# Kernel optimization log

Measured on AMD Instinct MI355X. Metric: run time of the kernel, lower is better.

## Reference

```python
import jax, jax.numpy as jnp
import numpy as np

B, L, D = 4, 4096, 1024
H, HD = 16, 64          # num_heads, head_dims
K = 256                 # Linformer low-rank dim
SCALE = HD ** -0.5


def setup_inputs() -> dict:
    key = jax.random.key(0)
    ks = jax.random.split(key, 7)
    std_d = 1.0 / np.sqrt(D)
    std_k = 1.0 / np.sqrt(K)
    return {
        "x": jax.random.normal(ks[0], (B, L, D), dtype=jnp.float32),
        "Wq": jax.random.uniform(ks[1], (D, D), jnp.float32, -std_d, std_d),
        "Wk": jax.random.uniform(ks[2], (D, D), jnp.float32, -std_d, std_d),
        "Wv": jax.random.uniform(ks[3], (D, D), jnp.float32, -std_d, std_d),
        "Wo": jax.random.uniform(ks[4], (D, D), jnp.float32, -std_d, std_d),
        "proj_k": jax.random.uniform(ks[5], (L, K), jnp.float32, -std_k, std_k),
        "proj_v": jax.random.uniform(ks[6], (L, K), jnp.float32, -std_k, std_k),
    }


def reference(x, Wq, Wk, Wv, Wo, proj_k, proj_v):
    # QKV projections (bias-free linears)
    q = x @ Wq                                   # [B, L, D]
    k = x @ Wk                                   # [B, L, D]
    v = x @ Wv                                   # [B, L, D]
    # Linformer low-rank projection along sequence: 'bld,lk->bkd'
    k = jnp.einsum('bld,lk->bkd', k, proj_k)     # [B, K, D]
    v = jnp.einsum('bld,lk->bkd', v, proj_v)     # [B, K, D]
    # split heads
    q = q.reshape(B, L, H, HD).transpose(0, 2, 1, 3)   # [B, H, L, HD]
    k = k.reshape(B, K, H, HD).transpose(0, 2, 1, 3)   # [B, H, K, HD]
    v = v.reshape(B, K, H, HD).transpose(0, 2, 1, 3)   # [B, H, K, HD]
    # attention over compressed length K
    logits = jnp.einsum('bhld,bhkd->bhlk', q, k) * SCALE   # [B, H, L, K]
    attn = jax.nn.softmax(logits, axis=-1)
    out = jnp.einsum('bhlk,bhkd->bhld', attn, v)           # [B, H, L, HD]
    out = out.transpose(0, 2, 1, 3).reshape(B, L, H * HD)  # [B, L, D]
    return out @ Wo
```

## Files before the change

kernel.cpp:

```cpp
#include <hip/hip_runtime.h>
#include <stdint.h>

typedef __bf16 bf16;
typedef __bf16 bf16x4 __attribute__((ext_vector_type(4)));
typedef __bf16 bf16x8 __attribute__((ext_vector_type(8)));
typedef float f32x4 __attribute__((ext_vector_type(4)));

__global__ __launch_bounds__(256) void k_castT(const float* __restrict__ src,
                                               bf16* __restrict__ dst,
                                               bf16* __restrict__ dstT) {
  const size_t bo = (size_t)blockIdx.z * 4096 * 1024;
  const float* s = src + bo;
  bf16* d = dst + bo;
  bf16* dT = dstT + bo;
  __shared__ float tile[64][65];
  const int r0 = blockIdx.y * 64, c0 = blockIdx.x * 64;
  const int tr = threadIdx.x >> 6, tc = threadIdx.x & 63;
#pragma unroll
  for (int i = 0; i < 16; ++i) {
    const int r = i * 4 + tr;
    const float v = s[(size_t)(r0 + r) * 1024 + (c0 + tc)];
    tile[r][tc] = v;
    d[(size_t)(r0 + r) * 1024 + (c0 + tc)] = (bf16)v;
  }
  __syncthreads();
#pragma unroll
  for (int i = 0; i < 16; ++i) {
    const int r = i * 4 + tr;
    dT[(size_t)(c0 + r) * 4096 + (r0 + tc)] = (bf16)tile[tc][r];
  }
}

struct TP4 { const float* src[4]; bf16* dst[4]; };

__global__ __launch_bounds__(256) void k_tcast(TP4 args, int R, int C) {
  const float* __restrict__ src = args.src[blockIdx.z];
  bf16* __restrict__ dst = args.dst[blockIdx.z];
  __shared__ float tile[64][65];
  const int r0 = blockIdx.y * 64, c0 = blockIdx.x * 64;
  const int tr = threadIdx.x >> 6, tc = threadIdx.x & 63;
#pragma unroll
  for (int i = 0; i < 16; ++i) {
    int r = i * 4 + tr;
    tile[r][tc] = src[(size_t)(r0 + r) * C + (c0 + tc)];
  }
  __syncthreads();
#pragma unroll
  for (int i = 0; i < 16; ++i) {
    int r = i * 4 + tr;
    dst[(size_t)(c0 + r) * R + (r0 + tc)] = (bf16)tile[tc][r];
  }
}

#define GLL(gp, lp)                                              \
  __builtin_amdgcn_global_load_lds(                              \
      (const __attribute__((address_space(1))) void*)(gp),       \
      (__attribute__((address_space(3))) void*)(lp), 16, 0, 0)

template <typename CT>
__global__ __launch_bounds__(256) void k_gemm_nt(
    const bf16* __restrict__ A, const bf16* __restrict__ Bt,
    const bf16* __restrict__ Bt2, CT* __restrict__ C,
    int lda, int ldb, int ldc, int Kd, long sA, long sB, long sC,
    int zmod, long kOff, int mbSplit, CT* __restrict__ Ct, long sCt, int ldct,
    int mbT) {
  int zb = blockIdx.z, kc = 0;
  if (zmod > 1) { zb = blockIdx.z / zmod; kc = blockIdx.z % zmod; }
  const int mb = blockIdx.x, nb = blockIdx.y;
  A += (long)zb * sA + (long)kc * kOff;
  const bf16* Bsel = (mb < mbSplit) ? Bt : Bt2;
  Bsel += (long)zb * sB + (long)kc * kOff;
  C += (long)blockIdx.z * sC;
  Ct += (long)blockIdx.z * sCt;

  __shared__ bf16 As[2][128 * 32];
  __shared__ bf16 Bs[2][128 * 32];
  const int tid = threadIdx.x, lane = tid & 63, wid = tid >> 6;
  const int wr = wid >> 1, wc = wid & 1;
  const int srow = lane >> 2;
  const int skk = (((lane & 3) ^ ((srow >> 1) & 3)) << 3);

  f32x4 acc[4][4] = {};
  const bf16* Abase = A + (long)mb * 128 * lda;
  const bf16* Bbase = Bsel + (long)nb * 128 * ldb;

  auto stage = [&](int buf, int k0) {
#pragma unroll
    for (int i = 0; i < 2; ++i) {
      const int ch = wid * 2 + i;
      const int row = ch * 16 + srow;
      GLL(Abase + (long)row * lda + k0 + skk, &As[buf][ch * 512]);
      GLL(Bbase + (long)row * ldb + k0 + skk, &Bs[buf][ch * 512]);
    }
  };

  stage(0, 0);
  const int nk = Kd >> 5;
  for (int kt = 0; kt < nk; ++kt) {
    const int cur = kt & 1;
    if (kt + 1 < nk) stage(cur ^ 1, (kt + 1) << 5);
    __syncthreads();
    const int slot = lane >> 4;
    bf16x8 af[4], bb[4];
#pragma unroll
    for (int i = 0; i < 4; ++i) {
      const int r = wr * 64 + i * 16 + (lane & 15);
      af[i] = *reinterpret_cast<const bf16x8*>(
          reinterpret_cast<const char*>(As[cur]) + r * 64 +
          ((slot ^ ((r >> 1) & 3)) << 4));
      const int c = wc * 64 + i * 16 + (lane & 15);
      bb[i] = *reinterpret_cast<const bf16x8*>(
          reinterpret_cast<const char*>(Bs[cur]) + c * 64 +
          ((slot ^ ((c >> 1) & 3)) << 4));
    }
#pragma unroll
    for (int i = 0; i < 4; ++i)
#pragma unroll
      for (int j = 0; j < 4; ++j)
        acc[i][j] =
            __builtin_amdgcn_mfma_f32_16x16x32_bf16(af[i], bb[j], acc[i][j], 0, 0, 0);
    __syncthreads();
  }

  const long row0 = (long)mb * 128 + wr * 64 + ((lane >> 4) << 2);
  const int col0 = nb * 128 + wc * 64 + (lane & 15);
  if (mb >= mbT) {
    const long r0 = row0 - (long)mbT * 128;
#pragma unroll
    for (int i = 0; i < 4; ++i)
#pragma unroll
      for (int j = 0; j < 4; ++j)
#pragma unroll
        for (int r = 0; r < 4; ++r)
          Ct[(long)(col0 + j * 16) * ldct + (r0 + i * 16 + r)] = (CT)acc[i][j][r];
  } else {
#pragma unroll
    for (int i = 0; i < 4; ++i)
#pragma unroll
      for (int j = 0; j < 4; ++j)
#pragma unroll
        for (int r = 0; r < 4; ++r)
          C[(row0 + i * 16 + r) * ldc + (col0 + j * 16)] = (CT)acc[i][j][r];
  }
}

__global__ __launch_bounds__(256) void k_red4(const float* __restrict__ p,
                                              bf16* __restrict__ out) {
  const int i = blockIdx.x * 256 + threadIdx.x;
  const int SL = 512 * 1024;
  const int b = (i * 4) / SL;
  const int e = (i * 4) % SL;
  const float* base = p + (size_t)b * 4 * SL + e;
  float4 s0 = *reinterpret_cast<const float4*>(base);
  float4 s1 = *reinterpret_cast<const float4*>(base + SL);
  float4 s2 = *reinterpret_cast<const float4*>(base + 2 * SL);
  float4 s3 = *reinterpret_cast<const float4*>(base + 3 * SL);
  bf16x4 o;
  o[0] = (bf16)(s0.x + s1.x + s2.x + s3.x);
  o[1] = (bf16)(s0.y + s1.y + s2.y + s3.y);
  o[2] = (bf16)(s0.z + s1.z + s2.z + s3.z);
  o[3] = (bf16)(s0.w + s1.w + s2.w + s3.w);
  *reinterpret_cast<bf16x4*>(out + (size_t)b * SL + e) = o;
}

__global__ __launch_bounds__(256) void k_attn(const bf16* __restrict__ q,
                                              const bf16* __restrict__ kc,
                                              const bf16* __restrict__ vT,
                                              bf16* __restrict__ aout) {
  const int lt = blockIdx.x, h = blockIdx.y, b = blockIdx.z;
  const int tid = threadIdx.x, lane = tid & 63, wid = tid >> 6;
  const int x = lane & 15, g = lane >> 4;
  __shared__ bf16 smem[32768];
  bf16* Ks = smem;
  bf16* Vs = smem + 16384;

  const bf16* kb = kc + ((long)b * 256) * 1024 + h * 64;
#pragma unroll
  for (int it = 0; it < 8; ++it) {
    const int lin = it * 256 + tid;
    const int k = lin >> 3, s = lin & 7;
    const int rel = k & 31;
    const int pk = (k & ~31) | ((rel & 1) << 4) | ((rel >> 3) << 2) | ((rel >> 1) & 3);
    bf16x8 v = *reinterpret_cast<const bf16x8*>(kb + (long)k * 1024 + s * 8);
    *reinterpret_cast<bf16x8*>(reinterpret_cast<char*>(Ks) + pk * 128 +
                               ((s ^ (pk & 7)) << 4)) = v;
  }
  const bf16* vb = vT + (long)b * 1024 * 256 + (long)h * 64 * 256;
#pragma unroll
  for (int it = 0; it < 8; ++it) {
    const int lin = it * 256 + tid;
    const int d = lin >> 5, s = lin & 31;
    bf16x8 v = *reinterpret_cast<const bf16x8*>(vb + (long)d * 256 + s * 8);
    *reinterpret_cast<bf16x8*>(reinterpret_cast<char*>(Vs) + d * 512 +
                               ((s ^ (d & 7)) << 4)) = v;
  }

  const long qrow0 = (long)b * 4096 + lt * 64 + wid * 16;
  const bf16* qb = q + (qrow0 + x) * 1024 + h * 64;
  bf16x8 qf[2];
#pragma unroll
  for (int ks2 = 0; ks2 < 2; ++ks2)
    qf[ks2] = *reinterpret_cast<const bf16x8*>(qb + ks2 * 32 + g * 8);

  __syncthreads();

  f32x4 ln[16] = {};
#pragma unroll
  for (int ks2 = 0; ks2 < 2; ++ks2) {
    const int slot = ks2 * 4 + g;
#pragma unroll
    for (int f = 0; f < 16; ++f) {
      const int row = f * 16 + x;
      bf16x8 kf = *reinterpret_cast<const bf16x8*>(
          reinterpret_cast<const char*>(Ks) + row * 128 + ((slot ^ (row & 7)) << 4));
      ln[f] = __builtin_amdgcn_mfma_f32_16x16x32_bf16(kf, qf[ks2], ln[f], 0, 0, 0);
    }
  }

  float m = -1e30f;
#pragma unroll
  for (int f = 0; f < 16; ++f)
#pragma unroll
    for (int r = 0; r < 4; ++r) m = fmaxf(m, ln[f][r]);
  m = fmaxf(m, __shfl_xor(m, 16, 64));
  m = fmaxf(m, __shfl_xor(m, 32, 64));
  float sum = 0.f;
#pragma unroll
  for (int f = 0; f < 16; ++f)
#pragma unroll
    for (int r = 0; r < 4; ++r) {
      const float p = __expf((ln[f][r] - m) * 0.125f);
      ln[f][r] = p;
      sum += p;
    }
  sum += __shfl_xor(sum, 16, 64);
  sum += __shfl_xor(sum, 32, 64);
  const float inv = 1.f / sum;

  f32x4 oacc[4] = {};
#pragma unroll
  for (int ks = 0; ks < 8; ++ks) {
    bf16x8 pa;
#pragma unroll
    for (int t = 0; t < 4; ++t) {
      pa[2 * t] = (bf16)ln[2 * ks][t];
      pa[2 * t + 1] = (bf16)ln[2 * ks + 1][t];
    }
    const int slot = ks * 4 + g;
#pragma unroll
    for (int nf = 0; nf < 4; ++nf) {
      const int d2 = nf * 16 + x;
      bf16x8 vv = *reinterpret_cast<const bf16x8*>(
          reinterpret_cast<const char*>(Vs) + d2 * 512 + ((slot ^ (d2 & 7)) << 4));
      oacc[nf] = __builtin_amdgcn_mfma_f32_16x16x32_bf16(pa, vv, oacc[nf], 0, 0, 0);
    }
  }

  float invr[4];
#pragma unroll
  for (int r = 0; r < 4; ++r) invr[r] = __shfl(inv, 4 * g + r, 64);
  bf16* ob = aout + (qrow0 + 4 * g) * 1024 + h * 64 + x;
#pragma unroll
  for (int nf = 0; nf < 4; ++nf)
#pragma unroll
    for (int r = 0; r < 4; ++r)
      ob[(long)r * 1024 + nf * 16] = (bf16)(oacc[nf][r] * invr[r]);
}

extern "C" void kernel_launch(void* const* d_in, const int* in_sizes, int n_in,
                              void* d_out, int out_size, void* d_ws, size_t ws_size,
                              hipStream_t stream) {
  const float* x  = (const float*)d_in[0];
  const float* Wq = (const float*)d_in[1];
  const float* Wk = (const float*)d_in[2];
  const float* Wv = (const float*)d_in[3];
  const float* Wo = (const float*)d_in[4];
  const float* Pk = (const float*)d_in[5];
  const float* Pv = (const float*)d_in[6];
  char* ws = (char*)d_ws;
  const long MB = 1024L * 1024;
  bf16* xbf = (bf16*)ws;
  bf16* XT  = (bf16*)(ws + 32 * MB);
  bf16* WqT = (bf16*)(ws + 64 * MB);
  bf16* WkT = (bf16*)(ws + 66 * MB);
  bf16* WvT = (bf16*)(ws + 68 * MB);
  bf16* WoT = (bf16*)(ws + 70 * MB);
  bf16* PT  = (bf16*)(ws + 72 * MB);
  float* XCp = (float*)(ws + 76 * MB);
  bf16* qbf = (bf16*)(ws + 76 * MB);
  bf16* XC  = (bf16*)(ws + 108 * MB);
  bf16* kcb = (bf16*)(ws + 112 * MB);
  bf16* vcT = (bf16*)(ws + 114 * MB);
  bf16* aout = xbf;
  const int BIG = 1 << 30;
  (void)in_sizes; (void)n_in; (void)out_size; (void)ws_size;

  k_castT<<<dim3(16, 64, 4), 256, 0, stream>>>(x, xbf, XT);

  TP4 tw = {{Wq, Wk, Wv, Wo}, {WqT, WkT, WvT, WoT}};
  k_tcast<<<dim3(16, 16, 4), 256, 0, stream>>>(tw, 1024, 1024);

  TP4 tp = {{Pk, Pv, Pk, Pk}, {PT, PT + 256 * 4096, PT, PT}};
  k_tcast<<<dim3(4, 64, 2), 256, 0, stream>>>(tp, 4096, 256);

  k_gemm_nt<float><<<dim3(4, 8, 16), 256, 0, stream>>>(
      PT, XT, XT, XCp, 4096, 4096, 1024, 1024, 0, 1024L * 4096, 512L * 1024, 4, 1024,
      BIG, XCp, 0, 1024, BIG);
  k_red4<<<dim3(2048), 256, 0, stream>>>(XCp, XC);

  k_gemm_nt<bf16><<<dim3(4, 8, 4), 256, 0, stream>>>(
      XC, WkT, WvT, kcb, 1024, 1024, 1024, 1024, 512L * 1024, 0, 256L * 1024, 1, 0, 2,
      vcT, 1024L * 256, 256, 2);

  k_gemm_nt<bf16><<<dim3(128, 8, 1), 256, 0, stream>>>(
      xbf, WqT, WqT, qbf, 1024, 1024, 1024, 1024, 0, 0, 0, 1, 0, BIG, qbf, 0, 1024,
      BIG);

  k_attn<<<dim3(64, 16, 4), 256, 0, stream>>>(qbf, kcb, vcT, aout);

  k_gemm_nt<float><<<dim3(128, 8, 1), 256, 0, stream>>>(
      aout, WoT, WoT, (float*)d_out, 1024, 1024, 1024, 1024, 0, 0, 0, 1, 0, BIG,
      (float*)d_out, 0, 1024, BIG);
}
```

Before: 225.0 us.

## Add 256x256-tile pipelined GEMM kernel for Q and output projections

```diff
diff --git a/kernel.cpp b/kernel.cpp
--- a/kernel.cpp
+++ b/kernel.cpp
@@ -142,6 +142,120 @@
         for (int r = 0; r < 4; ++r)
           C[(row0 + i * 16 + r) * ldc + (col0 + j * 16)] = (CT)acc[i][j][r];
   }
+}
+
+#define BARR __builtin_amdgcn_s_barrier()
+#define LGKM0                                             \
+  asm volatile("s_waitcnt lgkmcnt(0)" ::: "memory");      \
+  __builtin_amdgcn_sched_barrier(0)
+#define VMC(n)                                            \
+  asm volatile("s_waitcnt vmcnt(" #n ")" ::: "memory");   \
+  __builtin_amdgcn_sched_barrier(0)
+
+#define MFQ(q, AV)                                                            \
+  __builtin_amdgcn_s_setprio(1);                                              \
+  _Pragma("unroll") for (int i_ = 2 * (q); i_ < 2 * (q) + 2; ++i_)            \
+  _Pragma("unroll") for (int n_ = 0; n_ < 4; ++n_)                            \
+  _Pragma("unroll") for (int s_ = 0; s_ < 2; ++s_)                            \
+      acc[i_][n_] = __builtin_amdgcn_mfma_f32_16x16x32_bf16(                  \
+          AV[i_][s_], bv[n_][s_], acc[i_][n_], 0, 0, 0);                      \
+  __builtin_amdgcn_s_setprio(0)
+
+#define PHASES(t, CUR, AVC, AVN)                                              \
+  {                                                                           \
+    _Pragma("unroll") for (int n_ = 0; n_ < 4; ++n_)                          \
+    _Pragma("unroll") for (int s_ = 0; s_ < 2; ++s_)                          \
+        bv[n_][s_] = ldbf(CUR, n_, s_);                                       \
+    LGKM0;                                                                    \
+    BARR;                                                                     \
+    MFQ(0, AVC);                                                              \
+    _Pragma("unroll") for (int i_ = 4; i_ < 8; ++i_)                          \
+    _Pragma("unroll") for (int s_ = 0; s_ < 2; ++s_)                          \
+        AVC[i_][s_] = ldaf(CUR, i_, s_);                                      \
+    if ((t) + 2 < NT) stage(CUR, (t) + 2, 2);                                 \
+    MFQ(1, AVC);                                                              \
+    if ((t) + 2 < NT) stage(CUR, (t) + 2, 3);                                 \
+    LGKM0;                                                                    \
+    BARR;                                                                     \
+    MFQ(2, AVC);                                                              \
+    if ((t) + 2 < NT) { VMC(4); } else if ((t) + 1 < NT) { VMC(0); }          \
+    BARR;                                                                     \
+    if ((t) + 2 < NT) { stage(CUR, (t) + 2, 0); stage(CUR, (t) + 2, 1); }     \
+    if ((t) + 1 < NT)                                                         \
+      _Pragma("unroll") for (int i_ = 0; i_ < 4; ++i_)                        \
+      _Pragma("unroll") for (int s_ = 0; s_ < 2; ++s_)                        \
+          AVN[i_][s_] = ldaf((CUR) ^ 1, i_, s_);                              \
+    MFQ(3, AVC);                                                              \
+  }
+
+template <typename CT>
+__global__ __launch_bounds__(512, 2) void k_gemm256(
+    const bf16* __restrict__ A, const bf16* __restrict__ Bt, CT* __restrict__ C,
+    int NT) {
+  const int b0 = blockIdx.x;
+  const int swz = (b0 & 7) * 32 + (b0 >> 3);
+  const int mb = swz >> 2, nb = swz & 3;
+
+  const int tid = threadIdx.x, lane = tid & 63, wid = tid >> 6;
+  const int wr = wid >> 2, wc = wid & 3;
+  const int x = lane & 15, g = lane >> 4;
+  __shared__ bf16 Asl[2][16384];
+  __shared__ bf16 Bsl[2][16384];
+
+  const bf16* Ab = A + (long)mb * 256 * 1024;
+  const bf16* Bb = Bt + (long)nb * 256 * 1024;
+  const int srow8 = lane >> 3;
+  const int skk = (((lane & 7) ^ srow8) << 3);
+
+  auto stage = [&](int buf, int T, int j) {
+    const bf16* src = (j < 2) ? Ab : Bb;
+    bf16* db = ((j < 2) ? Asl[buf] : Bsl[buf]) + (j & 1) * 8192;
+    const long ko = (long)T * 64 + skk;
+#pragma unroll
+    for (int i2 = 0; i2 < 2; ++i2) {
+      const int c = wid * 2 + i2;
+      GLL(src + (long)((j & 1) * 128 + c * 8 + srow8) * 1024 + ko, db + c * 512);
+    }
+  };
+  auto ldaf = [&](int buf, int i, int s) {
+    const int r = wr * 128 + i * 16 + x;
+    return *reinterpret_cast<const bf16x8*>(
+        reinterpret_cast<const char*>(Asl[buf]) + r * 128 +
+        ((((s << 2) | g) ^ (r & 7)) << 4));
+  };
+  auto ldbf = [&](int buf, int n, int s) {
+    const int c = wc * 64 + n * 16 + x;
+    return *reinterpret_cast<const bf16x8*>(
+        reinterpret_cast<const char*>(Bsl[buf]) + c * 128 +
+        ((((s << 2) | g) ^ (c & 7)) << 4));
+  };
+
+  f32x4 acc[8][4] = {};
+  bf16x8 avA[8][2], avB[8][2], bv[4][2];
+
+  stage(0, 0, 2); stage(0, 0, 3); stage(0, 0, 0); stage(0, 0, 1);
+  stage(1, 1, 2); stage(1, 1, 3); stage(1, 1, 0); stage(1, 1, 1);
+  VMC(8);
+  BARR;
+#pragma unroll
+  for (int i_ = 0; i_ < 4; ++i_)
+#pragma unroll
+    for (int s_ = 0; s_ < 2; ++s_) avA[i_][s_] = ldaf(0, i_, s_);
+
+  for (int tt = 0; tt < NT; tt += 2) {
+    PHASES(tt, 0, avA, avB);
+    PHASES(tt + 1, 1, avB, avA);
+  }
+
+  const long row0 = (long)mb * 256 + wr * 128 + (g << 2);
+  const int col0 = nb * 256 + wc * 64 + x;
+#pragma unroll
+  for (int i = 0; i < 8; ++i)
+#pragma unroll
+    for (int n = 0; n < 4; ++n)
+#pragma unroll
+      for (int r = 0; r < 4; ++r)
+        C[(row0 + i * 16 + r) * 1024 + (col0 + n * 16)] = (CT)acc[i][n][r];
 }
 
 __global__ __launch_bounds__(256) void k_red4(const float* __restrict__ p,
@@ -312,13 +426,9 @@
       XC, WkT, WvT, kcb, 1024, 1024, 1024, 1024, 512L * 1024, 0, 256L * 1024, 1, 0, 2,
       vcT, 1024L * 256, 256, 2);
 
-  k_gemm_nt<bf16><<<dim3(128, 8, 1), 256, 0, stream>>>(
-      xbf, WqT, WqT, qbf, 1024, 1024, 1024, 1024, 0, 0, 0, 1, 0, BIG, qbf, 0, 1024,
-      BIG);
+  k_gemm256<bf16><<<dim3(256), 512, 0, stream>>>(xbf, WqT, qbf, 16);
 
   k_attn<<<dim3(64, 16, 4), 256, 0, stream>>>(qbf, kcb, vcT, aout);
 
-  k_gemm_nt<float><<<dim3(128, 8, 1), 256, 0, stream>>>(
-      aout, WoT, WoT, (float*)d_out, 1024, 1024, 1024, 1024, 0, 0, 0, 1, 0, BIG,
-      (float*)d_out, 0, 1024, BIG);
-}
+  k_gemm256<float><<<dim3(256), 512, 0, stream>>>(aout, WoT, (float*)d_out, 16);
+}
```

New measurement: 308.0 us. 1.37x slower.
